# Kernel tuning notes

Measured on AMD Instinct MI355X. Metric: run time of the kernel, lower is better.

The kernel has to match this reference:

```python
import jax, jax.numpy as jnp
import numpy as np
import math


def _instance_cl(z1, z2):
    # z1, z2: [B, T, C] -> per-element instance contrastive loss [B, T]
    B = z1.shape[0]
    z = jnp.concatenate([z1, z2], axis=0)          # [2B, T, C]
    z = z.transpose(1, 0, 2)                        # [T, 2B, C]
    sim = jnp.einsum('tic,tjc->tij', z, z)          # [T, 2B, 2B]
    # drop diagonal: tril(-1) shifted + triu(1) shifted -> [T, 2B, 2B-1]
    logits = jnp.tril(sim, -1)[:, :, :-1] + jnp.triu(sim, 1)[:, :, 1:]
    logits = -jax.nn.log_softmax(logits, axis=-1)
    i = jnp.arange(B)
    loss = (logits[:, i, B + i - 1] + logits[:, B + i, i]) / 2.0   # [T, B]
    return loss.T                                    # [B, T]


def _temporal_cl(z1, z2):
    # z1, z2: [B, T, C] -> per-timestep temporal contrastive loss [B, T]
    T = z1.shape[1]
    z = jnp.concatenate([z1, z2], axis=1)            # [B, 2T, C]
    sim = jnp.einsum('bic,bjc->bij', z, z)           # [B, 2T, 2T]
    logits = jnp.tril(sim, -1)[:, :, :-1] + jnp.triu(sim, 1)[:, :, 1:]
    logits = -jax.nn.log_softmax(logits, axis=-1)
    t = jnp.arange(T)
    return (logits[:, t, T + t - 1] + logits[:, T + t, t]) / 2.0   # [B, T]


def _contrastive_corr(z1, z2, alpha=0.5):
    # per-(batch, timestep) contrastive score, shape [B, L]
    return alpha * _instance_cl(z1, z2) + (1.0 - alpha) * _temporal_cl(z1, z2)


def setup_inputs() -> dict:
    key = jax.random.key(0)
    k1, k2, k3 = jax.random.split(key, 3)
    B, L, H, E = 4, 2048, 8, 64
    queries = jax.random.normal(k1, (B, L, H, E), dtype=jnp.float32)
    keys = jax.random.normal(k2, (B, L, H, E), dtype=jnp.float32)
    values = jax.random.normal(k3, (B, L, H, E), dtype=jnp.float32)
    attn_mask = jnp.zeros((1,), dtype=bool)  # unused; ProbMask is rebuilt internally
    return {"queries": queries, "keys": keys, "values": values, "attn_mask": attn_mask}


FACTOR = 1.0


def reference(queries, keys, values, attn_mask):
    B, L, H, E = queries.shape
    # S == L here so key/value slicing branch is a no-op
    corr = _contrastive_corr(queries.reshape(B, L, H * E),
                             keys.reshape(B, L, H * E))       # [B, L]
    top_k = int(FACTOR * math.log(L))                          # static (=7 for L=2048)
    _, index = jax.lax.top_k(corr.mean(axis=0), top_k)         # [K]
    corr_top = corr[:, index]                                  # [B, K]
    # scores[b,h,k,l] = corr_top[b,k] broadcast over h and l
    scores = jnp.broadcast_to(corr_top[:, None, :, None], (B, H, top_k, L))
    # ProbMask: mask future positions l > index[k] (causal for the selected queries)
    mask = jnp.arange(L)[None, :] > index[:, None]             # [K, L]
    scores = jnp.where(mask[None, None, :, :], -jnp.inf, scores)
    attn = jax.nn.softmax(scores, axis=-1)                     # [B, H, K, L]
    V = values.transpose(0, 2, 1, 3)                           # [B, H, L, D]
    context = jnp.cumsum(V, axis=2)                            # initial context (mask_flag=True)
    out = jnp.einsum('bhkl,bhld->bhkd', attn, V)               # [B, H, K, D]
    context = context.at[:, :, index, :].set(out)              # scatter update
    return context
```

## Files before the change

kernel.cpp:

```cpp
#include <hip/hip_runtime.h>
#include <math.h>


typedef __attribute__((ext_vector_type(8))) short short8;
typedef __attribute__((ext_vector_type(8))) unsigned short ushort8;
typedef __attribute__((ext_vector_type(4))) float f32x4;

typedef const __attribute__((address_space(1))) void* gas_ptr;
typedef __attribute__((address_space(3))) void* las_ptr;

#define EXP_OFF 80.0f

__device__ __forceinline__ void async_cp16(const void* g, void* l) {
  __builtin_amdgcn_global_load_lds((gas_ptr)g, (las_ptr)l, 16, 0, 0);
}

__device__ __forceinline__ unsigned short f2bf(float x) {
  union { float f; unsigned int u; } v; v.f = x;
  unsigned int r = v.u + 0x7FFFu + ((v.u >> 16) & 1u);
  return (unsigned short)(r >> 16);
}

__global__ __launch_bounds__(256) void convert_bf16_kernel(
    const float* __restrict__ Q, const float* __restrict__ K,
    unsigned short* __restrict__ Z) {
  int tid = blockIdx.x * 256 + threadIdx.x;
  int row = tid >> 6;
  int c0 = (tid & 63) * 8;
  int b = row >> 12, i = row & 4095;
  const float* src = (i < 2048)
      ? Q + ((size_t)(b * 2048 + i) * 512 + c0)
      : K + ((size_t)(b * 2048 + (i - 2048)) * 512 + c0);
  float4 v0 = ((const float4*)src)[0];
  float4 v1 = ((const float4*)src)[1];
  ushort8 o;
  o[0] = f2bf(v0.x); o[1] = f2bf(v0.y); o[2] = f2bf(v0.z); o[3] = f2bf(v0.w);
  o[4] = f2bf(v1.x); o[5] = f2bf(v1.y); o[6] = f2bf(v1.z); o[7] = f2bf(v1.w);
  *(ushort8*)(Z + (size_t)row * 512 + c0) = o;
}

__global__ __launch_bounds__(256, 3) void temporal_gemm_kernel(
    const unsigned short* __restrict__ Z, float* __restrict__ part) {
  int id = blockIdx.x;
  int x = id & 7;
  int b = x >> 1;
  int t = (id >> 3) * 2 + (x & 1);
  int cj = (int)((sqrtf(8.0f * (float)t + 1.0f) - 1.0f) * 0.5f);
  while ((cj + 1) * (cj + 2) / 2 <= t) cj++;
  while (cj * (cj + 1) / 2 > t) cj--;
  int ri = t - cj * (cj + 1) / 2;
  const unsigned short* Zb = Z + (size_t)b * 4096 * 512;

  __shared__ __align__(16) unsigned short As[2][128 * 32];
  __shared__ __align__(16) unsigned short Bs[2][128 * 32];

  int tid = threadIdx.x;
  int w = tid >> 6, lane = tid & 63;
  int wr = w >> 1, wc = w & 1;
  int lm = lane & 15, q = lane >> 4;
  int swz = q ^ ((lm >> 1) & 3);

  int srow = lane >> 2;
  int kq = (lane & 3) ^ ((lane >> 3) & 3);
  int rl0 = w * 16 + srow;
  int rl1 = 64 + rl0;
  const unsigned short* gA0 = Zb + (size_t)(ri * 128 + rl0) * 512 + kq * 8;
  const unsigned short* gA1 = Zb + (size_t)(ri * 128 + rl1) * 512 + kq * 8;
  const unsigned short* gB0 = Zb + (size_t)(cj * 128 + rl0) * 512 + kq * 8;
  const unsigned short* gB1 = Zb + (size_t)(cj * 128 + rl1) * 512 + kq * 8;
  int lo0 = (w * 16) * 32;
  int lo1 = (64 + w * 16) * 32;

  f32x4 acc[4][4];
#pragma unroll
  for (int mi = 0; mi < 4; mi++)
#pragma unroll
    for (int ni = 0; ni < 4; ni++) acc[mi][ni] = (f32x4)(0.f);

  async_cp16(gA0, As[0] + lo0);
  async_cp16(gA1, As[0] + lo1);
  async_cp16(gB0, Bs[0] + lo0);
  async_cp16(gB1, Bs[0] + lo1);

  for (int kc = 0; kc < 16; ++kc) {
    int cur = kc & 1;
    __syncthreads();

    if (kc < 15) {
      int go = (kc + 1) * 32;
      async_cp16(gA0 + go, As[cur ^ 1] + lo0);
      async_cp16(gA1 + go, As[cur ^ 1] + lo1);
      async_cp16(gB0 + go, Bs[cur ^ 1] + lo0);
      async_cp16(gB1 + go, Bs[cur ^ 1] + lo1);
    }

    short8 af[4], bfr[4];
#pragma unroll
    for (int mi = 0; mi < 4; mi++) {
      int ar = wr * 64 + mi * 16 + lm;
      af[mi] = *(const short8*)(As[cur] + ar * 32 + swz * 8);
    }
#pragma unroll
    for (int ni = 0; ni < 4; ni++) {
      int bc = wc * 64 + ni * 16 + lm;
      bfr[ni] = *(const short8*)(Bs[cur] + bc * 32 + swz * 8);
    }
#pragma unroll
    for (int mi = 0; mi < 4; mi++)
#pragma unroll
      for (int ni = 0; ni < 4; ni++)
        acc[mi][ni] = __builtin_amdgcn_mfma_f32_16x16x32_bf16(
            af[mi], bfr[ni], acc[mi][ni], 0, 0, 0);
  }

  float rsum[4][4];
  float csum[4];
#pragma unroll
  for (int mi = 0; mi < 4; mi++)
#pragma unroll
    for (int rr = 0; rr < 4; rr++) rsum[mi][rr] = 0.f;
#pragma unroll
  for (int ni = 0; ni < 4; ni++) csum[ni] = 0.f;

#pragma unroll
  for (int mi = 0; mi < 4; mi++) {
#pragma unroll
    for (int ni = 0; ni < 4; ni++) {
#pragma unroll
      for (int rr = 0; rr < 4; rr++) {
        int R = ri * 128 + wr * 64 + mi * 16 + q * 4 + rr;
        int Cg = cj * 128 + wc * 64 + ni * 16 + lm;
        float e = (R != Cg) ? __expf(acc[mi][ni][rr] - EXP_OFF) : 0.f;
        rsum[mi][rr] += e;
        csum[ni] += e;
      }
    }
  }

#pragma unroll
  for (int mi = 0; mi < 4; mi++) {
#pragma unroll
    for (int rr = 0; rr < 4; rr++) {
      float s = rsum[mi][rr];
      s += __shfl_xor(s, 1);
      s += __shfl_xor(s, 2);
      s += __shfl_xor(s, 4);
      s += __shfl_xor(s, 8);
      if (lm == 0) {
        int R = ri * 128 + wr * 64 + mi * 16 + q * 4 + rr;
        part[((size_t)(b * 4096 + R)) * 64 + cj * 2 + wc] = s;
      }
    }
  }

  if (ri != cj) {
#pragma unroll
    for (int ni = 0; ni < 4; ni++) {
      float s = csum[ni];
      s += __shfl_xor(s, 16);
      s += __shfl_xor(s, 32);
      if (q == 0) {
        int Cg = cj * 128 + wc * 64 + ni * 16 + lm;
        part[((size_t)(b * 4096 + Cg)) * 64 + ri * 2 + wr] = s;
      }
    }
  }
}

__global__ __launch_bounds__(256) void merge_row_kernel(
    const float* __restrict__ part, float* __restrict__ lse_temp) {
  int row = blockIdx.x * 256 + threadIdx.x;
  const float4* p = (const float4*)(part + (size_t)row * 64);
  float s = 0.f;
#pragma unroll
  for (int i = 0; i < 16; i++) {
    float4 v = p[i];
    s += v.x + v.y + v.z + v.w;
  }
  lse_temp[row] = EXP_OFF + __logf(s);
}

__global__ __launch_bounds__(256) void instance_kernel(
    const unsigned short* __restrict__ Z,
    float* __restrict__ lse_inst ,
    float* __restrict__ posdot ) {
  int wave = (blockIdx.x * 256 + threadIdx.x) >> 6;
  int t0 = wave * 2;
  int lane = threadIdx.x & 63;
  int lm = lane & 15, q = lane >> 4;
  int tt = (lm < 8) ? t0 : t0 + 1;
  int v = lm & 7;
  size_t zrow = (v < 4) ? ((size_t)v * 4096 + tt)
                        : ((size_t)(v - 4) * 4096 + 2048 + tt);
  const unsigned short* g = Z + zrow * 512 + q * 8;

  f32x4 acc0 = (f32x4)(0.f), acc1 = (f32x4)(0.f);
#pragma unroll
  for (int kc = 0; kc < 16; kc += 2) {
    short8 a0 = *(const short8*)(g + kc * 32);
    short8 a1 = *(const short8*)(g + kc * 32 + 32);
    acc0 = __builtin_amdgcn_mfma_f32_16x16x32_bf16(a0, a0, acc0, 0, 0, 0);
    acc1 = __builtin_amdgcn_mfma_f32_16x16x32_bf16(a1, a1, acc1, 0, 0, 0);
  }
  f32x4 acc = acc0 + acc1;

#pragma unroll
  for (int rr = 0; rr < 4; rr++) {
    int i = q * 4 + rr;
    float val = acc[rr];
    bool samehalf = ((i < 8) == (lm < 8));
    int t = (i < 8) ? t0 : t0 + 1;
    int iv = i & 7;
    if (samehalf && iv < 4 && (lm & 7) == iv + 4)
      posdot[iv * 2048 + t] = val;
    float dd = (samehalf && lm != i) ? val : -INFINITY;
    float mt = dd;
    mt = fmaxf(mt, __shfl_xor(mt, 1));
    mt = fmaxf(mt, __shfl_xor(mt, 2));
    mt = fmaxf(mt, __shfl_xor(mt, 4));
    float e = __expf(dd - mt);
    e += __shfl_xor(e, 1);
    e += __shfl_xor(e, 2);
    e += __shfl_xor(e, 4);
    if ((lm & 7) == 0 && samehalf) lse_inst[t * 8 + iv] = mt + __logf(e);
  }
}

__global__ __launch_bounds__(256) void combine_topk_kernel(
    const float* __restrict__ lse_inst, const float* __restrict__ lse_temp,
    const float* __restrict__ posdot, int* __restrict__ index_out) {
  __shared__ float wmax[4];
  __shared__ int widx[4];
  int tid = threadIdx.x;
  int base = tid * 8;
  float v[8];
#pragma unroll
  for (int r = 0; r < 8; r++) {
    int t = base + r;
    float sum = 0.f;
#pragma unroll
    for (int b = 0; b < 4; b++) {
      sum += 0.25f * (lse_inst[t * 8 + b] + lse_inst[t * 8 + 4 + b] +
                      lse_temp[b * 4096 + t] + lse_temp[b * 4096 + 2048 + t]) -
             posdot[b * 2048 + t];
    }
    v[r] = sum * 0.25f;
  }
  int lane = tid & 63, w = tid >> 6;
  for (int k = 0; k < 7; k++) {
    float bv = v[0];
    int bi = base;
#pragma unroll
    for (int r = 1; r < 8; r++)
      if (v[r] > bv) { bv = v[r]; bi = base + r; }
#pragma unroll
    for (int d = 1; d < 64; d <<= 1) {
      float ov = __shfl_xor(bv, d);
      int oi = __shfl_xor(bi, d);
      if (ov > bv || (ov == bv && oi < bi)) { bv = ov; bi = oi; }
    }
    if (lane == 0) { wmax[w] = bv; widx[w] = bi; }
    __syncthreads();
    float BV = wmax[0];
    int BI = widx[0];
#pragma unroll
    for (int ww = 1; ww < 4; ww++)
      if (wmax[ww] > BV || (wmax[ww] == BV && widx[ww] < BI)) {
        BV = wmax[ww];
        BI = widx[ww];
      }
    if (tid == 0) index_out[k] = BI;
    if (BI >= base && BI < base + 8) v[BI - base] = -INFINITY;
    __syncthreads();
  }
}

__global__ __launch_bounds__(1024) void cumsum_kernel(
    const float* __restrict__ V, const int* __restrict__ index,
    float* __restrict__ out) {
  int bh = blockIdx.x;
  int h = bh & 7, b = bh >> 3;
  int tid = threadIdx.x;
  int e = tid & 63, c = tid >> 6;
  __shared__ float psum[16][64];

  const float* Vbase = V + (size_t)(b * 2048) * 512 + h * 64 + e;
  float* obase = out + (size_t)bh * 2048 * 64 + e;

  int l0 = c * 128;
  float s = 0.f;
  for (int l = l0; l < l0 + 128; ++l) s += Vbase[(size_t)l * 512];
  psum[c][e] = s;

  int idx[7];
#pragma unroll
  for (int k = 0; k < 7; k++) idx[k] = index[k];
  __syncthreads();

  float run = 0.f;
#pragma unroll
  for (int cc = 0; cc < 16; ++cc) {
    float p = psum[cc][e];
    if (cc < c) run += p;
  }

  for (int l = l0; l < l0 + 128; ++l) {
    run += Vbase[(size_t)l * 512];
    float o = run;
    bool special = false;
#pragma unroll
    for (int k = 0; k < 7; k++) special = special || (idx[k] == l);
    if (special) o = run / (float)(l + 1);
    obase[(size_t)l * 64] = o;
  }
}

extern "C" void kernel_launch(void* const* d_in, const int* in_sizes, int n_in,
                              void* d_out, int out_size, void* d_ws, size_t ws_size,
                              hipStream_t stream) {
  const float* Q = (const float*)d_in[0];
  const float* K = (const float*)d_in[1];
  const float* V = (const float*)d_in[2];
  float* out = (float*)d_out;

  unsigned short* Z = (unsigned short*)d_ws;
  float* base = (float*)d_ws + 4 * 4096 * 512 / 2;
  float* part = base;
  float* lse_t = base + 4 * 4096 * 64;
  float* lse_i = lse_t + 16384;
  float* posd = lse_i + 16384;
  int* idx = (int*)(posd + 8192);

  convert_bf16_kernel<<<4096, 256, 0, stream>>>(Q, K, Z);
  temporal_gemm_kernel<<<4 * 528, 256, 0, stream>>>(Z, part);
  instance_kernel<<<256, 256, 0, stream>>>(Z, lse_i, posd);
  merge_row_kernel<<<64, 256, 0, stream>>>(part, lse_t);
  combine_topk_kernel<<<1, 256, 0, stream>>>(lse_i, lse_t, posd, idx);
  cumsum_kernel<<<32, 1024, 0, stream>>>(V, idx, out);
}
```

Before: 193.1 us.

## Fuse instance loss into conversion kernel and split cumsum across many blocks

The instance-contrastive computation moves into the bf16 conversion launch as extra blocks that read fp32 Q/K directly and convert in registers, removing one launch and its dependence on Z. The cumsum over V, previously run by only 32 blocks, is split into a partial-sum kernel and a write kernel with 512 blocks each, which spreads the memory-bound scan across far more CUs. The cost is an extra launch, a second pass over V, and a serial prefix loop over up to 63 partials per thread.

```diff
diff --git a/kernel.cpp b/kernel.cpp
--- a/kernel.cpp
+++ b/kernel.cpp
@@ -21,184 +21,52 @@
   return (unsigned short)(r >> 16);
 }
 
-__global__ __launch_bounds__(256) void convert_bf16_kernel(
+__global__ __launch_bounds__(256) void conv_inst_kernel(
     const float* __restrict__ Q, const float* __restrict__ K,
-    unsigned short* __restrict__ Z) {
-  int tid = blockIdx.x * 256 + threadIdx.x;
-  int row = tid >> 6;
-  int c0 = (tid & 63) * 8;
-  int b = row >> 12, i = row & 4095;
-  const float* src = (i < 2048)
-      ? Q + ((size_t)(b * 2048 + i) * 512 + c0)
-      : K + ((size_t)(b * 2048 + (i - 2048)) * 512 + c0);
-  float4 v0 = ((const float4*)src)[0];
-  float4 v1 = ((const float4*)src)[1];
-  ushort8 o;
-  o[0] = f2bf(v0.x); o[1] = f2bf(v0.y); o[2] = f2bf(v0.z); o[3] = f2bf(v0.w);
-  o[4] = f2bf(v1.x); o[5] = f2bf(v1.y); o[6] = f2bf(v1.z); o[7] = f2bf(v1.w);
-  *(ushort8*)(Z + (size_t)row * 512 + c0) = o;
-}
-
-__global__ __launch_bounds__(256, 3) void temporal_gemm_kernel(
-    const unsigned short* __restrict__ Z, float* __restrict__ part) {
-  int id = blockIdx.x;
-  int x = id & 7;
-  int b = x >> 1;
-  int t = (id >> 3) * 2 + (x & 1);
-  int cj = (int)((sqrtf(8.0f * (float)t + 1.0f) - 1.0f) * 0.5f);
-  while ((cj + 1) * (cj + 2) / 2 <= t) cj++;
-  while (cj * (cj + 1) / 2 > t) cj--;
-  int ri = t - cj * (cj + 1) / 2;
-  const unsigned short* Zb = Z + (size_t)b * 4096 * 512;
-
-  __shared__ __align__(16) unsigned short As[2][128 * 32];
-  __shared__ __align__(16) unsigned short Bs[2][128 * 32];
-
-  int tid = threadIdx.x;
-  int w = tid >> 6, lane = tid & 63;
-  int wr = w >> 1, wc = w & 1;
-  int lm = lane & 15, q = lane >> 4;
-  int swz = q ^ ((lm >> 1) & 3);
-
-  int srow = lane >> 2;
-  int kq = (lane & 3) ^ ((lane >> 3) & 3);
-  int rl0 = w * 16 + srow;
-  int rl1 = 64 + rl0;
-  const unsigned short* gA0 = Zb + (size_t)(ri * 128 + rl0) * 512 + kq * 8;
-  const unsigned short* gA1 = Zb + (size_t)(ri * 128 + rl1) * 512 + kq * 8;
-  const unsigned short* gB0 = Zb + (size_t)(cj * 128 + rl0) * 512 + kq * 8;
-  const unsigned short* gB1 = Zb + (size_t)(cj * 128 + rl1) * 512 + kq * 8;
-  int lo0 = (w * 16) * 32;
-  int lo1 = (64 + w * 16) * 32;
-
-  f32x4 acc[4][4];
-#pragma unroll
-  for (int mi = 0; mi < 4; mi++)
-#pragma unroll
-    for (int ni = 0; ni < 4; ni++) acc[mi][ni] = (f32x4)(0.f);
-
-  async_cp16(gA0, As[0] + lo0);
-  async_cp16(gA1, As[0] + lo1);
-  async_cp16(gB0, Bs[0] + lo0);
-  async_cp16(gB1, Bs[0] + lo1);
-
-  for (int kc = 0; kc < 16; ++kc) {
-    int cur = kc & 1;
-    __syncthreads();
-
-    if (kc < 15) {
-      int go = (kc + 1) * 32;
-      async_cp16(gA0 + go, As[cur ^ 1] + lo0);
-      async_cp16(gA1 + go, As[cur ^ 1] + lo1);
-      async_cp16(gB0 + go, Bs[cur ^ 1] + lo0);
-      async_cp16(gB1 + go, Bs[cur ^ 1] + lo1);
-    }
-
-    short8 af[4], bfr[4];
-#pragma unroll
-    for (int mi = 0; mi < 4; mi++) {
-      int ar = wr * 64 + mi * 16 + lm;
-      af[mi] = *(const short8*)(As[cur] + ar * 32 + swz * 8);
-    }
-#pragma unroll
-    for (int ni = 0; ni < 4; ni++) {
-      int bc = wc * 64 + ni * 16 + lm;
-      bfr[ni] = *(const short8*)(Bs[cur] + bc * 32 + swz * 8);
-    }
-#pragma unroll
-    for (int mi = 0; mi < 4; mi++)
-#pragma unroll
-      for (int ni = 0; ni < 4; ni++)
-        acc[mi][ni] = __builtin_amdgcn_mfma_f32_16x16x32_bf16(
-            af[mi], bfr[ni], acc[mi][ni], 0, 0, 0);
-  }
-
-  float rsum[4][4];
-  float csum[4];
-#pragma unroll
-  for (int mi = 0; mi < 4; mi++)
-#pragma unroll
-    for (int rr = 0; rr < 4; rr++) rsum[mi][rr] = 0.f;
-#pragma unroll
-  for (int ni = 0; ni < 4; ni++) csum[ni] = 0.f;
-
-#pragma unroll
-  for (int mi = 0; mi < 4; mi++) {
-#pragma unroll
-    for (int ni = 0; ni < 4; ni++) {
-#pragma unroll
-      for (int rr = 0; rr < 4; rr++) {
-        int R = ri * 128 + wr * 64 + mi * 16 + q * 4 + rr;
-        int Cg = cj * 128 + wc * 64 + ni * 16 + lm;
-        float e = (R != Cg) ? __expf(acc[mi][ni][rr] - EXP_OFF) : 0.f;
-        rsum[mi][rr] += e;
-        csum[ni] += e;
-      }
-    }
-  }
-
-#pragma unroll
-  for (int mi = 0; mi < 4; mi++) {
-#pragma unroll
-    for (int rr = 0; rr < 4; rr++) {
-      float s = rsum[mi][rr];
-      s += __shfl_xor(s, 1);
-      s += __shfl_xor(s, 2);
-      s += __shfl_xor(s, 4);
-      s += __shfl_xor(s, 8);
-      if (lm == 0) {
-        int R = ri * 128 + wr * 64 + mi * 16 + q * 4 + rr;
-        part[((size_t)(b * 4096 + R)) * 64 + cj * 2 + wc] = s;
-      }
-    }
-  }
-
-  if (ri != cj) {
-#pragma unroll
-    for (int ni = 0; ni < 4; ni++) {
-      float s = csum[ni];
-      s += __shfl_xor(s, 16);
-      s += __shfl_xor(s, 32);
-      if (q == 0) {
-        int Cg = cj * 128 + wc * 64 + ni * 16 + lm;
-        part[((size_t)(b * 4096 + Cg)) * 64 + ri * 2 + wr] = s;
-      }
-    }
-  }
-}
-
-__global__ __launch_bounds__(256) void merge_row_kernel(
-    const float* __restrict__ part, float* __restrict__ lse_temp) {
-  int row = blockIdx.x * 256 + threadIdx.x;
-  const float4* p = (const float4*)(part + (size_t)row * 64);
-  float s = 0.f;
-#pragma unroll
-  for (int i = 0; i < 16; i++) {
-    float4 v = p[i];
-    s += v.x + v.y + v.z + v.w;
-  }
-  lse_temp[row] = EXP_OFF + __logf(s);
-}
-
-__global__ __launch_bounds__(256) void instance_kernel(
-    const unsigned short* __restrict__ Z,
+    unsigned short* __restrict__ Z,
     float* __restrict__ lse_inst ,
     float* __restrict__ posdot ) {
-  int wave = (blockIdx.x * 256 + threadIdx.x) >> 6;
+  if (blockIdx.x < 4096) {
+    int tid = blockIdx.x * 256 + threadIdx.x;
+    int row = tid >> 6;
+    int c0 = (tid & 63) * 8;
+    int b = row >> 12, i = row & 4095;
+    const float* src = (i < 2048)
+        ? Q + ((size_t)(b * 2048 + i) * 512 + c0)
+        : K + ((size_t)(b * 2048 + (i - 2048)) * 512 + c0);
+    float4 v0 = ((const float4*)src)[0];
+    float4 v1 = ((const float4*)src)[1];
+    ushort8 o;
+    o[0] = f2bf(v0.x); o[1] = f2bf(v0.y); o[2] = f2bf(v0.z); o[3] = f2bf(v0.w);
+    o[4] = f2bf(v1.x); o[5] = f2bf(v1.y); o[6] = f2bf(v1.z); o[7] = f2bf(v1.w);
+    *(ushort8*)(Z + (size_t)row * 512 + c0) = o;
+    return;
+  }
+  int wave = ((blockIdx.x - 4096) * 256 + threadIdx.x) >> 6;
   int t0 = wave * 2;
   int lane = threadIdx.x & 63;
   int lm = lane & 15, q = lane >> 4;
   int tt = (lm < 8) ? t0 : t0 + 1;
   int v = lm & 7;
-  size_t zrow = (v < 4) ? ((size_t)v * 4096 + tt)
-                        : ((size_t)(v - 4) * 4096 + 2048 + tt);
-  const unsigned short* g = Z + zrow * 512 + q * 8;
+  const float* g = ((v < 4) ? Q + ((size_t)v * 2048 + tt) * 512
+                            : K + ((size_t)(v - 4) * 2048 + tt) * 512) + q * 8;
 
   f32x4 acc0 = (f32x4)(0.f), acc1 = (f32x4)(0.f);
 #pragma unroll
   for (int kc = 0; kc < 16; kc += 2) {
-    short8 a0 = *(const short8*)(g + kc * 32);
-    short8 a1 = *(const short8*)(g + kc * 32 + 32);
+    float4 x0 = ((const float4*)(g + kc * 32))[0];
+    float4 x1 = ((const float4*)(g + kc * 32))[1];
+    float4 y0 = ((const float4*)(g + kc * 32 + 32))[0];
+    float4 y1 = ((const float4*)(g + kc * 32 + 32))[1];
+    short8 a0, a1;
+    a0[0] = (short)f2bf(x0.x); a0[1] = (short)f2bf(x0.y);
+    a0[2] = (short)f2bf(x0.z); a0[3] = (short)f2bf(x0.w);
+    a0[4] = (short)f2bf(x1.x); a0[5] = (short)f2bf(x1.y);
+    a0[6] = (short)f2bf(x1.z); a0[7] = (short)f2bf(x1.w);
+    a1[0] = (short)f2bf(y0.x); a1[1] = (short)f2bf(y0.y);
+    a1[2] = (short)f2bf(y0.z); a1[3] = (short)f2bf(y0.w);
+    a1[4] = (short)f2bf(y1.x); a1[5] = (short)f2bf(y1.y);
+    a1[6] = (short)f2bf(y1.z); a1[7] = (short)f2bf(y1.w);
     acc0 = __builtin_amdgcn_mfma_f32_16x16x32_bf16(a0, a0, acc0, 0, 0, 0);
     acc1 = __builtin_amdgcn_mfma_f32_16x16x32_bf16(a1, a1, acc1, 0, 0, 0);
   }
@@ -226,6 +94,147 @@
   }
 }
 
+__global__ __launch_bounds__(256, 3) void temporal_gemm_kernel(
+    const unsigned short* __restrict__ Z, float* __restrict__ part) {
+  int id = blockIdx.x;
+  int x = id & 7;
+  int b = x >> 1;
+  int t = (id >> 3) * 2 + (x & 1);
+  int cj = (int)((sqrtf(8.0f * (float)t + 1.0f) - 1.0f) * 0.5f);
+  while ((cj + 1) * (cj + 2) / 2 <= t) cj++;
+  while (cj * (cj + 1) / 2 > t) cj--;
+  int ri = t - cj * (cj + 1) / 2;
+  const unsigned short* Zb = Z + (size_t)b * 4096 * 512;
+
+  __shared__ __align__(16) unsigned short As[2][128 * 32];
+  __shared__ __align__(16) unsigned short Bs[2][128 * 32];
+
+  int tid = threadIdx.x;
+  int w = tid >> 6, lane = tid & 63;
+  int wr = w >> 1, wc = w & 1;
+  int lm = lane & 15, q = lane >> 4;
+  int swz = q ^ ((lm >> 1) & 3);
+
+  int srow = lane >> 2;
+  int kq = (lane & 3) ^ ((lane >> 3) & 3);
+  int rl0 = w * 16 + srow;
+  int rl1 = 64 + rl0;
+  const unsigned short* gA0 = Zb + (size_t)(ri * 128 + rl0) * 512 + kq * 8;
+  const unsigned short* gA1 = Zb + (size_t)(ri * 128 + rl1) * 512 + kq * 8;
+  const unsigned short* gB0 = Zb + (size_t)(cj * 128 + rl0) * 512 + kq * 8;
+  const unsigned short* gB1 = Zb + (size_t)(cj * 128 + rl1) * 512 + kq * 8;
+  int lo0 = (w * 16) * 32;
+  int lo1 = (64 + w * 16) * 32;
+
+  f32x4 acc[4][4];
+#pragma unroll
+  for (int mi = 0; mi < 4; mi++)
+#pragma unroll
+    for (int ni = 0; ni < 4; ni++) acc[mi][ni] = (f32x4)(0.f);
+
+  async_cp16(gA0, As[0] + lo0);
+  async_cp16(gA1, As[0] + lo1);
+  async_cp16(gB0, Bs[0] + lo0);
+  async_cp16(gB1, Bs[0] + lo1);
+
+  for (int kc = 0; kc < 16; ++kc) {
+    int cur = kc & 1;
+    __syncthreads();
+
+    if (kc < 15) {
+      int go = (kc + 1) * 32;
+      async_cp16(gA0 + go, As[cur ^ 1] + lo0);
+      async_cp16(gA1 + go, As[cur ^ 1] + lo1);
+      async_cp16(gB0 + go, Bs[cur ^ 1] + lo0);
+      async_cp16(gB1 + go, Bs[cur ^ 1] + lo1);
+    }
+
+    short8 af[4], bfr[4];
+#pragma unroll
+    for (int mi = 0; mi < 4; mi++) {
+      int ar = wr * 64 + mi * 16 + lm;
+      af[mi] = *(const short8*)(As[cur] + ar * 32 + swz * 8);
+    }
+#pragma unroll
+    for (int ni = 0; ni < 4; ni++) {
+      int bc = wc * 64 + ni * 16 + lm;
+      bfr[ni] = *(const short8*)(Bs[cur] + bc * 32 + swz * 8);
+    }
+#pragma unroll
+    for (int mi = 0; mi < 4; mi++)
+#pragma unroll
+      for (int ni = 0; ni < 4; ni++)
+        acc[mi][ni] = __builtin_amdgcn_mfma_f32_16x16x32_bf16(
+            af[mi], bfr[ni], acc[mi][ni], 0, 0, 0);
+  }
+
+  float rsum[4][4];
+  float csum[4];
+#pragma unroll
+  for (int mi = 0; mi < 4; mi++)
+#pragma unroll
+    for (int rr = 0; rr < 4; rr++) rsum[mi][rr] = 0.f;
+#pragma unroll
+  for (int ni = 0; ni < 4; ni++) csum[ni] = 0.f;
+
+#pragma unroll
+  for (int mi = 0; mi < 4; mi++) {
+#pragma unroll
+    for (int ni = 0; ni < 4; ni++) {
+#pragma unroll
+      for (int rr = 0; rr < 4; rr++) {
+        int R = ri * 128 + wr * 64 + mi * 16 + q * 4 + rr;
+        int Cg = cj * 128 + wc * 64 + ni * 16 + lm;
+        float e = (R != Cg) ? __expf(acc[mi][ni][rr] - EXP_OFF) : 0.f;
+        rsum[mi][rr] += e;
+        csum[ni] += e;
+      }
+    }
+  }
+
+#pragma unroll
+  for (int mi = 0; mi < 4; mi++) {
+#pragma unroll
+    for (int rr = 0; rr < 4; rr++) {
+      float s = rsum[mi][rr];
+      s += __shfl_xor(s, 1);
+      s += __shfl_xor(s, 2);
+      s += __shfl_xor(s, 4);
+      s += __shfl_xor(s, 8);
+      if (lm == 0) {
+        int R = ri * 128 + wr * 64 + mi * 16 + q * 4 + rr;
+        part[((size_t)(b * 4096 + R)) * 64 + cj * 2 + wc] = s;
+      }
+    }
+  }
+
+  if (ri != cj) {
+#pragma unroll
+    for (int ni = 0; ni < 4; ni++) {
+      float s = csum[ni];
+      s += __shfl_xor(s, 16);
+      s += __shfl_xor(s, 32);
+      if (q == 0) {
+        int Cg = cj * 128 + wc * 64 + ni * 16 + lm;
+        part[((size_t)(b * 4096 + Cg)) * 64 + ri * 2 + wr] = s;
+      }
+    }
+  }
+}
+
+__global__ __launch_bounds__(256) void merge_row_kernel(
+    const float* __restrict__ part, float* __restrict__ lse_temp) {
+  int row = blockIdx.x * 256 + threadIdx.x;
+  const float4* p = (const float4*)(part + (size_t)row * 64);
+  float s = 0.f;
+#pragma unroll
+  for (int i = 0; i < 16; i++) {
+    float4 v = p[i];
+    s += v.x + v.y + v.z + v.w;
+  }
+  lse_temp[row] = EXP_OFF + __logf(s);
+}
+
 __global__ __launch_bounds__(256) void combine_topk_kernel(
     const float* __restrict__ lse_inst, const float* __restrict__ lse_temp,
     const float* __restrict__ posdot, int* __restrict__ index_out) {
@@ -275,43 +284,49 @@
   }
 }
 
-__global__ __launch_bounds__(1024) void cumsum_kernel(
-    const float* __restrict__ V, const int* __restrict__ index,
-    float* __restrict__ out) {
-  int bh = blockIdx.x;
+__global__ __launch_bounds__(256) void cumsum_part_kernel(
+    const float* __restrict__ V, float* __restrict__ spart) {
+  int blk = blockIdx.x;
+  int chunk = blk & 15, bh = blk >> 4;
   int h = bh & 7, b = bh >> 3;
   int tid = threadIdx.x;
-  int e = tid & 63, c = tid >> 6;
-  __shared__ float psum[16][64];
-
-  const float* Vbase = V + (size_t)(b * 2048) * 512 + h * 64 + e;
-  float* obase = out + (size_t)bh * 2048 * 64 + e;
-
-  int l0 = c * 128;
+  int e = tid & 63, sub = tid >> 6;
+  const float* Vb = V + (size_t)b * 1048576 + h * 64 + e;
+  int l0 = chunk * 128 + sub * 32;
   float s = 0.f;
-  for (int l = l0; l < l0 + 128; ++l) s += Vbase[(size_t)l * 512];
-  psum[c][e] = s;
+  for (int l = l0; l < l0 + 32; ++l) s += Vb[(size_t)l * 512];
+  spart[(size_t)(bh * 64 + chunk * 4 + sub) * 64 + e] = s;
+}
+
+__global__ __launch_bounds__(256) void cumsum_write_kernel(
+    const float* __restrict__ V, const float* __restrict__ spart,
+    const int* __restrict__ index, float* __restrict__ out) {
+  int blk = blockIdx.x;
+  int chunk = blk & 15, bh = blk >> 4;
+  int h = bh & 7, b = bh >> 3;
+  int tid = threadIdx.x;
+  int e = tid & 63, sub = tid >> 6;
+  const float* Vb = V + (size_t)b * 1048576 + h * 64 + e;
+  float* ob = out + (size_t)bh * 131072 + e;
+
+  int lin = chunk * 4 + sub;
+  float run = 0.f;
+  for (int p = 0; p < lin; ++p)
+    run += spart[(size_t)(bh * 64 + p) * 64 + e];
 
   int idx[7];
 #pragma unroll
   for (int k = 0; k < 7; k++) idx[k] = index[k];
-  __syncthreads();
-
-  float run = 0.f;
-#pragma unroll
-  for (int cc = 0; cc < 16; ++cc) {
-    float p = psum[cc][e];
-    if (cc < c) run += p;
-  }
-
-  for (int l = l0; l < l0 + 128; ++l) {
-    run += Vbase[(size_t)l * 512];
+
+  int l0 = chunk * 128 + sub * 32;
+  for (int l = l0; l < l0 + 32; ++l) {
+    run += Vb[(size_t)l * 512];
     float o = run;
     bool special = false;
 #pragma unroll
     for (int k = 0; k < 7; k++) special = special || (idx[k] == l);
     if (special) o = run / (float)(l + 1);
-    obase[(size_t)l * 64] = o;
+    ob[(size_t)l * 64] = o;
   }
 }
 
@@ -330,11 +345,12 @@
   float* lse_i = lse_t + 16384;
   float* posd = lse_i + 16384;
   int* idx = (int*)(posd + 8192);
-
-  convert_bf16_kernel<<<4096, 256, 0, stream>>>(Q, K, Z);
+  float* spart = posd + 8192 + 8;
+
+  conv_inst_kernel<<<4096 + 256, 256, 0, stream>>>(Q, K, Z, lse_i, posd);
   temporal_gemm_kernel<<<4 * 528, 256, 0, stream>>>(Z, part);
-  instance_kernel<<<256, 256, 0, stream>>>(Z, lse_i, posd);
   merge_row_kernel<<<64, 256, 0, stream>>>(part, lse_t);
   combine_topk_kernel<<<1, 256, 0, stream>>>(lse_i, lse_t, posd, idx);
-  cumsum_kernel<<<32, 1024, 0, stream>>>(V, idx, out);
-}
+  cumsum_part_kernel<<<512, 256, 0, stream>>>(V, spart);
+  cumsum_write_kernel<<<512, 256, 0, stream>>>(V, spart, idx, out);
+}
```

After: 210.4 us. +9.0%, slower.
